# Performance work log

Measured on AMD Instinct MI355X. Metric: run time of the kernel, lower is better.

## Reference

```python
import jax, jax.numpy as jnp
import numpy as np

N_NODES = 100000
N_EDGES = 1600000
IN_DIM = 256
OUT_DIM = 128


def setup_inputs() -> dict:
    key = jax.random.key(0)
    k1, k2, k3, k4, k5 = jax.random.split(key, 5)
    h = jax.random.normal(k1, (N_NODES, IN_DIM), dtype=jnp.float32)
    # xavier_normal-ish scales for the two weight matrices
    W = jax.random.normal(k2, (IN_DIM, OUT_DIM), dtype=jnp.float32) * (2.0 / np.sqrt(IN_DIM + OUT_DIM))
    a = jax.random.normal(k3, (2 * OUT_DIM,), dtype=jnp.float32) * (2.0 / np.sqrt(2 * OUT_DIM + 1))
    src = jax.random.randint(k4, (N_EDGES,), 0, N_NODES, dtype=jnp.int32)
    dst = jax.random.randint(k5, (N_EDGES,), 0, N_NODES, dtype=jnp.int32)
    return {"h": h, "W": W, "a": a, "src": src, "dst": dst}


def reference(h, W, a, src, dst):
    n = h.shape[0]
    d = W.shape[1]
    z = h @ W  # [N, out_dim]
    # attn_fc([z_src || z_dst]) == z_src @ a[:d] + z_dst @ a[d:]
    el = z @ a[:d]  # [N]
    er = z @ a[d:]  # [N]
    e = jax.nn.leaky_relu(el[src] + er[dst])  # [E], torch default slope 0.01
    # per-destination (segment) softmax, numerically stable
    seg_max = jax.ops.segment_max(e, dst, num_segments=n)
    e_exp = jnp.exp(e - seg_max[dst])
    denom = jax.ops.segment_sum(e_exp, dst, num_segments=n)
    alpha = e_exp / denom[dst]  # [E]
    # weighted scatter-sum of source z into destinations
    h_out = jax.ops.segment_sum(alpha[:, None] * z[src], dst, num_segments=n)
    return h_out
```

## Files before the change

kernel.cpp:

```cpp
#include <hip/hip_runtime.h>
#include <cstdint>
#include <cstddef>

#define N_NODES 100000
#define N_EDGES 1600000
#define IN_DIM  256
#define OUT_DIM 128

#define BSHIFT 7
#define BNODES 128
#define NBUCK  782
#define BCAP   3200
#define MAXE   13
#define EPB    2048

#define ENC_NEG_INF 0x00800000u

typedef __attribute__((ext_vector_type(8))) short bf16x8;
typedef __attribute__((ext_vector_type(4))) float f32x4;

__device__ __forceinline__ unsigned bf16rn(float f) {
    unsigned u = __float_as_uint(f);
    return (u + 0x7FFFu + ((u >> 16) & 1u)) >> 16;
}

__global__ void w16s_k(const float* __restrict__ W, unsigned short* __restrict__ w16s,
                       int* __restrict__ bucket_cursor)
{
    int t = blockIdx.x * blockDim.x + threadIdx.x;
    if (t < NBUCK) bucket_cursor[t] = 0;
    if (t >= IN_DIM * OUT_DIM) return;
    int j  = t & 7;
    int n  = (t >> 3) & 15;
    int q  = (t >> 7) & 3;
    int c  = (t >> 9) & 7;
    int kc = t >> 12;
    int k   = kc * 32 + q * 8 + j;
    int dim = (c >> 1) * 32 + n * 2 + (c & 1);
    w16s[t] = (unsigned short)bf16rn(W[k * OUT_DIM + dim]);
}

#define LA_STRIDE 264

__global__ __launch_bounds__(256) void gemm_z_k(
    const float* __restrict__ h, const unsigned short* __restrict__ w16s,
    const float* __restrict__ a,
    unsigned short* __restrict__ z16, float* __restrict__ el, float* __restrict__ er)
{
    __shared__ unsigned short lA[64 * LA_STRIDE];
    const int t  = threadIdx.x;
    const int n0 = blockIdx.x * 64;

    #pragma unroll
    for (int p = 0; p < 16; ++p) {
        int f = p * 256 + t;
        int i = f >> 6;
        int col = (f & 63) * 4;
        float4 v = make_float4(0.f, 0.f, 0.f, 0.f);
        if (n0 + i < N_NODES)
            v = *(const float4*)&h[(size_t)(n0 + i) * IN_DIM + col];
        uint2 pk;
        pk.x = bf16rn(v.x) | (bf16rn(v.y) << 16);
        pk.y = bf16rn(v.z) | (bf16rn(v.w) << 16);
        *(uint2*)&lA[i * LA_STRIDE + col] = pk;
    }
    __syncthreads();

    const int w    = t >> 6;
    const int lane = t & 63;
    const int q    = lane >> 4;
    const int col  = lane & 15;

    f32x4 acc[8];
    #pragma unroll
    for (int c = 0; c < 8; ++c) acc[c] = (f32x4){0.f, 0.f, 0.f, 0.f};

    #pragma unroll
    for (int kc = 0; kc < 8; ++kc) {
        bf16x8 af = *(const bf16x8*)&lA[(w * 16 + col) * LA_STRIDE + kc * 32 + q * 8];
        bf16x8 bfr[8];
        #pragma unroll
        for (int c = 0; c < 8; ++c)
            bfr[c] = *(const bf16x8*)&w16s[((((kc * 8 + c) * 4 + q) * 16) + col) * 8];
        #pragma unroll
        for (int c = 0; c < 8; ++c)
            acc[c] = __builtin_amdgcn_mfma_f32_16x16x32_bf16(af, bfr[c], acc[c], 0, 0, 0);
    }

    float aL[8], aR[8];
    #pragma unroll
    for (int c = 0; c < 8; ++c) {
        int dim = (c >> 1) * 32 + col * 2 + (c & 1);
        aL[c] = a[dim];
        aR[c] = a[128 + dim];
    }
    #pragma unroll
    for (int r = 0; r < 4; ++r) {
        int node = n0 + w * 16 + q * 4 + r;
        float sl = 0.f, sr = 0.f;
        #pragma unroll
        for (int c = 0; c < 8; ++c) {
            sl += acc[c][r] * aL[c];
            sr += acc[c][r] * aR[c];
        }
        #pragma unroll
        for (int o = 1; o < 16; o <<= 1) {
            sl += __shfl_xor(sl, o, 64);
            sr += __shfl_xor(sr, o, 64);
        }
        if (node < N_NODES) {
            #pragma unroll
            for (int g = 0; g < 4; ++g) {
                unsigned u = bf16rn(acc[2 * g][r]) | (bf16rn(acc[2 * g + 1][r]) << 16);
                ((unsigned*)z16)[(size_t)node * 64 + g * 16 + col] = u;
            }
            if (col == 0) { el[node] = sl; er[node] = sr; }
        }
    }
}

__global__ __launch_bounds__(256) void partition_k(
    const int* __restrict__ src, const int* __restrict__ dst,
    const float* __restrict__ el, const float* __restrict__ er,
    int* __restrict__ bucket_cursor, unsigned long long* __restrict__ ebuf)
{
    __shared__ int hist[NBUCK];
    __shared__ int gbaseL[NBUCK];
    const int t = threadIdx.x;
    for (int i = t; i < NBUCK; i += 256) hist[i] = 0;
    __syncthreads();

    const int e0 = blockIdx.x * EPB;
    int bucks[8], ranks[8];
    unsigned long long pk[8];
    #pragma unroll
    for (int k = 0; k < 8; ++k) {
        int e = e0 + k * 256 + t;
        bucks[k] = -1;
        if (e < N_EDGES) {
            int s = src[e], d = dst[e];
            float v = el[s] + er[d];
            v = (v > 0.0f) ? v : 0.01f * v;
            int b = d >> BSHIFT;
            bucks[k] = b;
            ranks[k] = atomicAdd(&hist[b], 1);
            pk[k] = ((unsigned long long)__float_as_uint(v) << 32)
                  | ((unsigned)s << BSHIFT) | (unsigned)(d & (BNODES - 1));
        }
    }
    __syncthreads();
    for (int i = t; i < NBUCK; i += 256) {
        int hc = hist[i];
        gbaseL[i] = hc ? atomicAdd(&bucket_cursor[i], hc) : 0;
    }
    __syncthreads();
    #pragma unroll
    for (int k = 0; k < 8; ++k)
        if (bucks[k] >= 0)
            ebuf[(size_t)bucks[k] * BCAP + gbaseL[bucks[k]] + ranks[k]] = pk[k];
}

__global__ __launch_bounds__(256) void bucket_k(
    const int* __restrict__ bucket_cursor, const unsigned long long* __restrict__ ebuf,
    unsigned long long* __restrict__ perm, int* __restrict__ begA, int* __restrict__ endA)
{
    __shared__ int deg[BNODES];
    __shared__ int off[BNODES];
    __shared__ unsigned emaxL[BNODES];
    __shared__ int ssum[BNODES];

    const int b = blockIdx.x;
    const int t = threadIdx.x;
    const int cnt = bucket_cursor[b];
    const unsigned long long* eb = ebuf + (size_t)b * BCAP;
    unsigned long long* pb = perm + (size_t)b * BCAP;

    if (t < BNODES) { deg[t] = 0; emaxL[t] = ENC_NEG_INF; }
    __syncthreads();

    unsigned long long pv[MAXE];
    int rk[MAXE];
    #pragma unroll
    for (int k = 0; k < MAXE; ++k) {
        int i = t + k * 256;
        if (i < cnt) {
            unsigned long long v = eb[i];
            int ld = (int)(v & (BNODES - 1));
            unsigned e32 = (unsigned)(v >> 32);
            unsigned enc = (e32 & 0x80000000u) ? ~e32 : (e32 | 0x80000000u);
            rk[k] = atomicAdd(&deg[ld], 1);
            atomicMax(&emaxL[ld], enc);
            pv[k] = v;
        }
    }
    __syncthreads();

    int d = 0, pd = 0;
    if (t < BNODES) {
        d  = deg[t];
        pd = (d + 3) & ~3;
        ssum[t] = pd;
    }
    __syncthreads();
    #pragma unroll
    for (int o = 1; o < BNODES; o <<= 1) {
        int v = 0;
        if (t >= o && t < BNODES) v = ssum[t - o];
        __syncthreads();
        if (t < BNODES) ssum[t] += v;
        __syncthreads();
    }
    if (t < BNODES) off[t] = ssum[t] - pd;
    __syncthreads();

    #pragma unroll
    for (int k = 0; k < MAXE; ++k) {
        int i = t + k * 256;
        if (i < cnt) {
            unsigned long long v = pv[k];
            int ld = (int)(v & (BNODES - 1));
            unsigned s = (unsigned)((v >> BSHIFT) & 0x1FFFFu);
            float e = __uint_as_float((unsigned)(v >> 32));
            unsigned u = emaxL[ld];
            float mx = (u & 0x80000000u) ? __uint_as_float(u ^ 0x80000000u)
                                         : __uint_as_float(~u);
            float w = __expf(e - mx);
            pb[off[ld] + rk[k]] = ((unsigned long long)__float_as_uint(w) << 32) | s;
        }
    }

    if (t < BNODES) {
        int n = b * BNODES + t;
        if (n < N_NODES) {
            int o  = off[t];
            int gb = b * BCAP + o;
            begA[n] = gb;
            endA[n] = gb + pd;
            for (int j = o + d; j < o + pd; ++j) pb[j] = 0ull;
        }
    }
}

__global__ __launch_bounds__(256) void node_pass_k(
    const int* __restrict__ begA, const int* __restrict__ endA,
    const unsigned long long* __restrict__ perm,
    const unsigned* __restrict__ z16, float* __restrict__ out)
{
    int n    = (blockIdx.x * blockDim.x + threadIdx.x) >> 6;
    int lane = threadIdx.x & 63;
    if (n >= N_NODES) return;
    int beg = begA[n], end = endA[n];

    float acc0 = 0.0f, acc1 = 0.0f;
    if (end > beg) {
        float dsum = 0.0f;
        const uint4* pp = (const uint4*)perm;
        #pragma unroll 2
        for (int i = (beg >> 2); i < (end >> 2); ++i) {
            uint4 pA = pp[2 * i];
            uint4 pB = pp[2 * i + 1];
            unsigned q0 = z16[(size_t)pA.x * 64 + lane];
            unsigned q1 = z16[(size_t)pA.z * 64 + lane];
            unsigned q2 = z16[(size_t)pB.x * 64 + lane];
            unsigned q3 = z16[(size_t)pB.z * 64 + lane];
            float w0 = __uint_as_float(pA.y);
            float w1 = __uint_as_float(pA.w);
            float w2 = __uint_as_float(pB.y);
            float w3 = __uint_as_float(pB.w);
            acc0 += w0 * __uint_as_float(q0 << 16)
                  + w1 * __uint_as_float(q1 << 16)
                  + w2 * __uint_as_float(q2 << 16)
                  + w3 * __uint_as_float(q3 << 16);
            acc1 += w0 * __uint_as_float(q0 & 0xFFFF0000u)
                  + w1 * __uint_as_float(q1 & 0xFFFF0000u)
                  + w2 * __uint_as_float(q2 & 0xFFFF0000u)
                  + w3 * __uint_as_float(q3 & 0xFFFF0000u);
            dsum += w0 + w1 + w2 + w3;
        }
        float inv = 1.0f / dsum;
        acc0 *= inv; acc1 *= inv;
    }
    *(float2*)&out[(size_t)n * OUT_DIM + lane * 2] = make_float2(acc0, acc1);
}

extern "C" void kernel_launch(void* const* d_in, const int* in_sizes, int n_in,
                              void* d_out, int out_size, void* d_ws, size_t ws_size,
                              hipStream_t stream)
{
    (void)in_sizes; (void)n_in; (void)out_size; (void)ws_size;
    const float* h = (const float*)d_in[0];
    const float* W = (const float*)d_in[1];
    const float* a = (const float*)d_in[2];
    const int* src = (const int*)d_in[3];
    const int* dst = (const int*)d_in[4];
    float* out = (float*)d_out;

    char* ws = (char*)d_ws;
    size_t off = 0;
    auto alloc = [&](size_t bytes) -> char* {
        char* p = ws + off;
        off += (bytes + 255) & ~(size_t)255;
        return p;
    };
    unsigned short* z16  = (unsigned short*)alloc((size_t)N_NODES * OUT_DIM * 2);
    unsigned short* w16s = (unsigned short*)alloc((size_t)IN_DIM * OUT_DIM * 2);
    float*    el        = (float*)   alloc((size_t)N_NODES * 4);
    float*    er        = (float*)   alloc((size_t)N_NODES * 4);
    int*      bucket_cursor = (int*) alloc((size_t)NBUCK * 4);
    unsigned long long* ebuf = (unsigned long long*)alloc((size_t)NBUCK * BCAP * 8);
    unsigned long long* perm = (unsigned long long*)alloc((size_t)NBUCK * BCAP * 8);
    int*      begA      = (int*)     alloc((size_t)N_NODES * 4);
    int*      endA      = (int*)     alloc((size_t)N_NODES * 4);

    w16s_k<<<(IN_DIM * OUT_DIM + 255) / 256, 256, 0, stream>>>(W, w16s, bucket_cursor);
    gemm_z_k<<<(N_NODES + 63) / 64, 256, 0, stream>>>(h, w16s, a, z16, el, er);
    partition_k<<<(N_EDGES + EPB - 1) / EPB, 256, 0, stream>>>(src, dst, el, er,
                                                               bucket_cursor, ebuf);
    bucket_k<<<NBUCK, 256, 0, stream>>>(bucket_cursor, ebuf, perm, begA, endA);
    node_pass_k<<<(N_NODES * 64 + 255) / 256, 256, 0, stream>>>(begA, endA, perm,
                                                                (const unsigned*)z16, out);
}
```

Baseline: 314.2 us.

## Build destination CSR via global degree scan and atomic scatter

Replaces the two-level bucket partition (per-block histograms, bucket buffer, per-bucket sort) with a global CSR build. Per-destination degrees are counted with global atomics, prefix-scanned in two levels, and edges are then scattered into padded rows using an atomic cursor, with the segment max tracked by an atomicMax on an order-preserving encoding. The exp(e - max) is moved into the node aggregation pass, which removes the bucket kernel and its intermediate buffer. The GEMM also drops its LDS staging and loads and converts h straight into MFMA fragments. In exchange, each edge now needs several random global atomics and a scattered write, each lane recomputes the exp, and edge order within a row becomes nondeterministic.

Result: slower. 468.4 us (+49.1%).

```diff
diff --git a/kernel.cpp b/kernel.cpp
--- a/kernel.cpp
+++ b/kernel.cpp
@@ -7,14 +7,8 @@
 #define IN_DIM  256
 #define OUT_DIM 128
 
-#define BSHIFT 7
-#define BNODES 128
-#define NBUCK  782
-#define BCAP   3200
-#define MAXE   13
-#define EPB    2048
-
-#define ENC_NEG_INF 0x00800000u
+#define NSB 391
+#define PERM_CAP (N_EDGES + 4 * N_NODES)
 
 typedef __attribute__((ext_vector_type(8))) short bf16x8;
 typedef __attribute__((ext_vector_type(4))) float f32x4;
@@ -24,11 +18,12 @@
     return (u + 0x7FFFu + ((u >> 16) & 1u)) >> 16;
 }
 
-__global__ void w16s_k(const float* __restrict__ W, unsigned short* __restrict__ w16s,
-                       int* __restrict__ bucket_cursor)
+__global__ __launch_bounds__(256) void setup_k(
+    const float* __restrict__ W, unsigned short* __restrict__ w16s,
+    int* __restrict__ deg, unsigned* __restrict__ emaxEnc)
 {
     int t = blockIdx.x * blockDim.x + threadIdx.x;
-    if (t < NBUCK) bucket_cursor[t] = 0;
+    if (t < N_NODES) { deg[t] = 0; emaxEnc[t] = 0u; }
     if (t >= IN_DIM * OUT_DIM) return;
     int j  = t & 7;
     int n  = (t >> 3) & 15;
@@ -40,51 +35,107 @@
     w16s[t] = (unsigned short)bf16rn(W[k * OUT_DIM + dim]);
 }
 
-#define LA_STRIDE 264
+__global__ __launch_bounds__(256) void deg_k(const int* __restrict__ dst,
+                                             int* __restrict__ deg)
+{
+    int e0 = blockIdx.x * 1024 + threadIdx.x;
+    #pragma unroll
+    for (int k = 0; k < 4; ++k) {
+        int e = e0 + k * 256;
+        if (e < N_EDGES) atomicAdd(&deg[dst[e]], 1);
+    }
+}
+
+__global__ __launch_bounds__(256) void scan1_k(const int* __restrict__ deg,
+                                               int* __restrict__ nodeoff,
+                                               int* __restrict__ blocksum)
+{
+    __shared__ int s[256];
+    int b = blockIdx.x, t = threadIdx.x;
+    int n = b * 256 + t;
+    int d  = (n < N_NODES) ? deg[n] : 0;
+    int pd = (d + 3) & ~3;
+    s[t] = pd;
+    __syncthreads();
+    #pragma unroll
+    for (int o = 1; o < 256; o <<= 1) {
+        int v = (t >= o) ? s[t - o] : 0;
+        __syncthreads();
+        s[t] += v;
+        __syncthreads();
+    }
+    if (n < N_NODES) nodeoff[n] = s[t] - pd;
+    if (t == 255) blocksum[b] = s[255];
+}
+
+__global__ __launch_bounds__(512) void scan2_k(int* __restrict__ blocksum)
+{
+    __shared__ int s[512];
+    int t = threadIdx.x;
+    int v = (t < NSB) ? blocksum[t] : 0;
+    s[t] = v;
+    __syncthreads();
+    #pragma unroll
+    for (int o = 1; o < 512; o <<= 1) {
+        int x = (t >= o) ? s[t - o] : 0;
+        __syncthreads();
+        s[t] += x;
+        __syncthreads();
+    }
+    if (t < NSB) blocksum[t] = s[t] - v;
+}
+
+__global__ __launch_bounds__(256) void fixup_k(
+    const int* __restrict__ deg, const int* __restrict__ nodeoff,
+    const int* __restrict__ blocksum, int* __restrict__ begA, int* __restrict__ endA,
+    int* __restrict__ cur, unsigned long long* __restrict__ perm)
+{
+    int n = blockIdx.x * 256 + threadIdx.x;
+    if (n >= N_NODES) return;
+    int d  = deg[n];
+    int pd = (d + 3) & ~3;
+    int base = blocksum[n >> 8] + nodeoff[n];
+    begA[n] = base;
+    cur[n]  = base;
+    endA[n] = base + pd;
+    unsigned long long padv = ((unsigned long long)__float_as_uint(-1e30f)) << 32;
+    for (int j = base + d; j < base + pd; ++j) perm[j] = padv;
+}
 
 __global__ __launch_bounds__(256) void gemm_z_k(
     const float* __restrict__ h, const unsigned short* __restrict__ w16s,
     const float* __restrict__ a,
     unsigned short* __restrict__ z16, float* __restrict__ el, float* __restrict__ er)
 {
-    __shared__ unsigned short lA[64 * LA_STRIDE];
-    const int t  = threadIdx.x;
-    const int n0 = blockIdx.x * 64;
-
-    #pragma unroll
-    for (int p = 0; p < 16; ++p) {
-        int f = p * 256 + t;
-        int i = f >> 6;
-        int col = (f & 63) * 4;
-        float4 v = make_float4(0.f, 0.f, 0.f, 0.f);
-        if (n0 + i < N_NODES)
-            v = *(const float4*)&h[(size_t)(n0 + i) * IN_DIM + col];
-        uint2 pk;
-        pk.x = bf16rn(v.x) | (bf16rn(v.y) << 16);
-        pk.y = bf16rn(v.z) | (bf16rn(v.w) << 16);
-        *(uint2*)&lA[i * LA_STRIDE + col] = pk;
-    }
-    __syncthreads();
-
+    const int t    = threadIdx.x;
+    const int n0   = blockIdx.x * 64;
     const int w    = t >> 6;
     const int lane = t & 63;
     const int q    = lane >> 4;
     const int col  = lane & 15;
 
+    int row  = n0 + w * 16 + col;
+    int lrow = (row < N_NODES) ? row : (N_NODES - 1);
+    const float* hp = h + (size_t)lrow * IN_DIM + q * 8;
+
     f32x4 acc[8];
     #pragma unroll
     for (int c = 0; c < 8; ++c) acc[c] = (f32x4){0.f, 0.f, 0.f, 0.f};
 
     #pragma unroll
     for (int kc = 0; kc < 8; ++kc) {
-        bf16x8 af = *(const bf16x8*)&lA[(w * 16 + col) * LA_STRIDE + kc * 32 + q * 8];
-        bf16x8 bfr[8];
+        float4 v0 = *(const float4*)(hp + kc * 32);
+        float4 v1 = *(const float4*)(hp + kc * 32 + 4);
+        bf16x8 af;
+        af[0] = (short)bf16rn(v0.x); af[1] = (short)bf16rn(v0.y);
+        af[2] = (short)bf16rn(v0.z); af[3] = (short)bf16rn(v0.w);
+        af[4] = (short)bf16rn(v1.x); af[5] = (short)bf16rn(v1.y);
+        af[6] = (short)bf16rn(v1.z); af[7] = (short)bf16rn(v1.w);
         #pragma unroll
-        for (int c = 0; c < 8; ++c)
-            bfr[c] = *(const bf16x8*)&w16s[((((kc * 8 + c) * 4 + q) * 16) + col) * 8];
-        #pragma unroll
-        for (int c = 0; c < 8; ++c)
-            acc[c] = __builtin_amdgcn_mfma_f32_16x16x32_bf16(af, bfr[c], acc[c], 0, 0, 0);
+        for (int c = 0; c < 8; ++c) {
+            bf16x8 bfr = *(const bf16x8*)&w16s[((((kc * 8 + c) * 4 + q) * 16) + col) * 8];
+            acc[c] = __builtin_amdgcn_mfma_f32_16x16x32_bf16(af, bfr, acc[c], 0, 0, 0);
+        }
     }
 
     float aL[8], aR[8];
@@ -119,131 +170,32 @@
     }
 }
 
-__global__ __launch_bounds__(256) void partition_k(
+__global__ __launch_bounds__(256) void scatter_k(
     const int* __restrict__ src, const int* __restrict__ dst,
     const float* __restrict__ el, const float* __restrict__ er,
-    int* __restrict__ bucket_cursor, unsigned long long* __restrict__ ebuf)
-{
-    __shared__ int hist[NBUCK];
-    __shared__ int gbaseL[NBUCK];
-    const int t = threadIdx.x;
-    for (int i = t; i < NBUCK; i += 256) hist[i] = 0;
-    __syncthreads();
-
-    const int e0 = blockIdx.x * EPB;
-    int bucks[8], ranks[8];
-    unsigned long long pk[8];
-    #pragma unroll
-    for (int k = 0; k < 8; ++k) {
-        int e = e0 + k * 256 + t;
-        bucks[k] = -1;
+    int* __restrict__ cur, unsigned* __restrict__ emaxEnc,
+    unsigned long long* __restrict__ perm)
+{
+    int e0 = blockIdx.x * 1024 + threadIdx.x;
+    #pragma unroll
+    for (int k = 0; k < 4; ++k) {
+        int e = e0 + k * 256;
         if (e < N_EDGES) {
             int s = src[e], d = dst[e];
             float v = el[s] + er[d];
             v = (v > 0.0f) ? v : 0.01f * v;
-            int b = d >> BSHIFT;
-            bucks[k] = b;
-            ranks[k] = atomicAdd(&hist[b], 1);
-            pk[k] = ((unsigned long long)__float_as_uint(v) << 32)
-                  | ((unsigned)s << BSHIFT) | (unsigned)(d & (BNODES - 1));
-        }
-    }
-    __syncthreads();
-    for (int i = t; i < NBUCK; i += 256) {
-        int hc = hist[i];
-        gbaseL[i] = hc ? atomicAdd(&bucket_cursor[i], hc) : 0;
-    }
-    __syncthreads();
-    #pragma unroll
-    for (int k = 0; k < 8; ++k)
-        if (bucks[k] >= 0)
-            ebuf[(size_t)bucks[k] * BCAP + gbaseL[bucks[k]] + ranks[k]] = pk[k];
-}
-
-__global__ __launch_bounds__(256) void bucket_k(
-    const int* __restrict__ bucket_cursor, const unsigned long long* __restrict__ ebuf,
-    unsigned long long* __restrict__ perm, int* __restrict__ begA, int* __restrict__ endA)
-{
-    __shared__ int deg[BNODES];
-    __shared__ int off[BNODES];
-    __shared__ unsigned emaxL[BNODES];
-    __shared__ int ssum[BNODES];
-
-    const int b = blockIdx.x;
-    const int t = threadIdx.x;
-    const int cnt = bucket_cursor[b];
-    const unsigned long long* eb = ebuf + (size_t)b * BCAP;
-    unsigned long long* pb = perm + (size_t)b * BCAP;
-
-    if (t < BNODES) { deg[t] = 0; emaxL[t] = ENC_NEG_INF; }
-    __syncthreads();
-
-    unsigned long long pv[MAXE];
-    int rk[MAXE];
-    #pragma unroll
-    for (int k = 0; k < MAXE; ++k) {
-        int i = t + k * 256;
-        if (i < cnt) {
-            unsigned long long v = eb[i];
-            int ld = (int)(v & (BNODES - 1));
-            unsigned e32 = (unsigned)(v >> 32);
-            unsigned enc = (e32 & 0x80000000u) ? ~e32 : (e32 | 0x80000000u);
-            rk[k] = atomicAdd(&deg[ld], 1);
-            atomicMax(&emaxL[ld], enc);
-            pv[k] = v;
-        }
-    }
-    __syncthreads();
-
-    int d = 0, pd = 0;
-    if (t < BNODES) {
-        d  = deg[t];
-        pd = (d + 3) & ~3;
-        ssum[t] = pd;
-    }
-    __syncthreads();
-    #pragma unroll
-    for (int o = 1; o < BNODES; o <<= 1) {
-        int v = 0;
-        if (t >= o && t < BNODES) v = ssum[t - o];
-        __syncthreads();
-        if (t < BNODES) ssum[t] += v;
-        __syncthreads();
-    }
-    if (t < BNODES) off[t] = ssum[t] - pd;
-    __syncthreads();
-
-    #pragma unroll
-    for (int k = 0; k < MAXE; ++k) {
-        int i = t + k * 256;
-        if (i < cnt) {
-            unsigned long long v = pv[k];
-            int ld = (int)(v & (BNODES - 1));
-            unsigned s = (unsigned)((v >> BSHIFT) & 0x1FFFFu);
-            float e = __uint_as_float((unsigned)(v >> 32));
-            unsigned u = emaxL[ld];
-            float mx = (u & 0x80000000u) ? __uint_as_float(u ^ 0x80000000u)
-                                         : __uint_as_float(~u);
-            float w = __expf(e - mx);
-            pb[off[ld] + rk[k]] = ((unsigned long long)__float_as_uint(w) << 32) | s;
-        }
-    }
-
-    if (t < BNODES) {
-        int n = b * BNODES + t;
-        if (n < N_NODES) {
-            int o  = off[t];
-            int gb = b * BCAP + o;
-            begA[n] = gb;
-            endA[n] = gb + pd;
-            for (int j = o + d; j < o + pd; ++j) pb[j] = 0ull;
+            unsigned u = __float_as_uint(v);
+            unsigned enc = (u >> 31) ? ~u : (u | 0x80000000u);
+            atomicMax(&emaxEnc[d], enc);
+            int p = atomicAdd(&cur[d], 1);
+            perm[(size_t)p] = ((unsigned long long)u << 32) | (unsigned)s;
         }
     }
 }
 
 __global__ __launch_bounds__(256) void node_pass_k(
     const int* __restrict__ begA, const int* __restrict__ endA,
-    const unsigned long long* __restrict__ perm,
+    const unsigned* __restrict__ emaxEnc, const unsigned long long* __restrict__ perm,
     const unsigned* __restrict__ z16, float* __restrict__ out)
 {
     int n    = (blockIdx.x * blockDim.x + threadIdx.x) >> 6;
@@ -253,6 +205,9 @@
 
     float acc0 = 0.0f, acc1 = 0.0f;
     if (end > beg) {
+        unsigned um = emaxEnc[n];
+        float mx = (um & 0x80000000u) ? __uint_as_float(um ^ 0x80000000u)
+                                      : __uint_as_float(~um);
         float dsum = 0.0f;
         const uint4* pp = (const uint4*)perm;
         #pragma unroll 2
@@ -263,10 +218,10 @@
             unsigned q1 = z16[(size_t)pA.z * 64 + lane];
             unsigned q2 = z16[(size_t)pB.x * 64 + lane];
             unsigned q3 = z16[(size_t)pB.z * 64 + lane];
-            float w0 = __uint_as_float(pA.y);
-            float w1 = __uint_as_float(pA.w);
-            float w2 = __uint_as_float(pB.y);
-            float w3 = __uint_as_float(pB.w);
+            float w0 = __expf(__uint_as_float(pA.y) - mx);
+            float w1 = __expf(__uint_as_float(pA.w) - mx);
+            float w2 = __expf(__uint_as_float(pB.y) - mx);
+            float w3 = __expf(__uint_as_float(pB.w) - mx);
             acc0 += w0 * __uint_as_float(q0 << 16)
                   + w1 * __uint_as_float(q1 << 16)
                   + w2 * __uint_as_float(q2 << 16)
@@ -306,17 +261,25 @@
     unsigned short* w16s = (unsigned short*)alloc((size_t)IN_DIM * OUT_DIM * 2);
     float*    el        = (float*)   alloc((size_t)N_NODES * 4);
     float*    er        = (float*)   alloc((size_t)N_NODES * 4);
-    int*      bucket_cursor = (int*) alloc((size_t)NBUCK * 4);
-    unsigned long long* ebuf = (unsigned long long*)alloc((size_t)NBUCK * BCAP * 8);
-    unsigned long long* perm = (unsigned long long*)alloc((size_t)NBUCK * BCAP * 8);
+    int*      deg       = (int*)     alloc((size_t)N_NODES * 4);
+    int*      nodeoff   = (int*)     alloc((size_t)N_NODES * 4);
+    int*      blocksum  = (int*)     alloc((size_t)NSB * 4);
     int*      begA      = (int*)     alloc((size_t)N_NODES * 4);
     int*      endA      = (int*)     alloc((size_t)N_NODES * 4);
-
-    w16s_k<<<(IN_DIM * OUT_DIM + 255) / 256, 256, 0, stream>>>(W, w16s, bucket_cursor);
+    int*      cur       = (int*)     alloc((size_t)N_NODES * 4);
+    unsigned* emaxEnc   = (unsigned*)alloc((size_t)N_NODES * 4);
+    unsigned long long* perm = (unsigned long long*)alloc((size_t)PERM_CAP * 8);
+
+    setup_k<<<(N_NODES + 255) / 256, 256, 0, stream>>>(W, w16s, deg, emaxEnc);
+    deg_k<<<(N_EDGES + 1023) / 1024, 256, 0, stream>>>(dst, deg);
+    scan1_k<<<NSB, 256, 0, stream>>>(deg, nodeoff, blocksum);
+    scan2_k<<<1, 512, 0, stream>>>(blocksum);
+    fixup_k<<<(N_NODES + 255) / 256, 256, 0, stream>>>(deg, nodeoff, blocksum,
+                                                       begA, endA, cur, perm);
     gemm_z_k<<<(N_NODES + 63) / 64, 256, 0, stream>>>(h, w16s, a, z16, el, er);
-    partition_k<<<(N_EDGES + EPB - 1) / EPB, 256, 0, stream>>>(src, dst, el, er,
-                                                               bucket_cursor, ebuf);
-    bucket_k<<<NBUCK, 256, 0, stream>>>(bucket_cursor, ebuf, perm, begA, endA);
-    node_pass_k<<<(N_NODES * 64 + 255) / 256, 256, 0, stream>>>(begA, endA, perm,
-                                                                (const unsigned*)z16, out);
-}
+    scatter_k<<<(N_EDGES + 1023) / 1024, 256, 0, stream>>>(src, dst, el, er,
+                                                           cur, emaxEnc, perm);
+    node_pass_k<<<(N_NODES * 64 + 255) / 256, 256, 0, stream>>>(begA, endA, emaxEnc,
+                                                                perm, (const unsigned*)z16,
+                                                                out);
+}
```

## Fuse bucket sort with node aggregation in LDS and defer edge scores

Applied to the files above, without the earlier changes.

Merges the bucket-sort and node-pass kernels so each bucket's sorted weights and source indices stay in shared memory instead of round-tripping through global perm/beg/end arrays. Edge scores are now computed from el/er inside the fused kernel, which halves the partition buffer width and lets partition run before the GEMM. The GEMM reads h directly into registers without LDS staging, and the prefix scan uses wave shuffles. The trade-off is much lower parallelism in the gather phase: each wave aggregates 32 nodes serially across only 782 blocks.

Result: no change. 308.3 us (-1.9%).

```diff
diff --git a/kernel.cpp b/kernel.cpp
--- a/kernel.cpp
+++ b/kernel.cpp
@@ -13,6 +13,7 @@
 #define BCAP   3200
 #define MAXE   13
 #define EPB    2048
+#define LCAP   3584
 
 #define ENC_NEG_INF 0x00800000u
 
@@ -23,9 +24,18 @@
     unsigned u = __float_as_uint(f);
     return (u + 0x7FFFu + ((u >> 16) & 1u)) >> 16;
 }
-
-__global__ void w16s_k(const float* __restrict__ W, unsigned short* __restrict__ w16s,
-                       int* __restrict__ bucket_cursor)
+__device__ __forceinline__ unsigned encOrd(float e) {
+    unsigned u = __float_as_uint(e);
+    return (u >> 31) ? ~u : (u | 0x80000000u);
+}
+__device__ __forceinline__ float decOrd(unsigned um) {
+    return (um & 0x80000000u) ? __uint_as_float(um ^ 0x80000000u)
+                              : __uint_as_float(~um);
+}
+
+__global__ __launch_bounds__(256) void setup_k(
+    const float* __restrict__ W, unsigned short* __restrict__ w16s,
+    int* __restrict__ bucket_cursor)
 {
     int t = blockIdx.x * blockDim.x + threadIdx.x;
     if (t < NBUCK) bucket_cursor[t] = 0;
@@ -40,51 +50,77 @@
     w16s[t] = (unsigned short)bf16rn(W[k * OUT_DIM + dim]);
 }
 
-#define LA_STRIDE 264
+__global__ __launch_bounds__(256) void partition_k(
+    const int* __restrict__ src, const int* __restrict__ dst,
+    int* __restrict__ bucket_cursor, unsigned* __restrict__ ebuf)
+{
+    __shared__ int hist[NBUCK];
+    __shared__ int gbaseL[NBUCK];
+    const int t = threadIdx.x;
+    for (int i = t; i < NBUCK; i += 256) hist[i] = 0;
+    __syncthreads();
+
+    const int e0 = blockIdx.x * EPB;
+    int bucks[8], ranks[8];
+    unsigned pk[8];
+    #pragma unroll
+    for (int k = 0; k < 8; ++k) {
+        int e = e0 + k * 256 + t;
+        bucks[k] = -1;
+        if (e < N_EDGES) {
+            int s = src[e], d = dst[e];
+            int b = d >> BSHIFT;
+            bucks[k] = b;
+            ranks[k] = atomicAdd(&hist[b], 1);
+            pk[k] = ((unsigned)s << BSHIFT) | (unsigned)(d & (BNODES - 1));
+        }
+    }
+    __syncthreads();
+    for (int i = t; i < NBUCK; i += 256) {
+        int hc = hist[i];
+        gbaseL[i] = hc ? atomicAdd(&bucket_cursor[i], hc) : 0;
+    }
+    __syncthreads();
+    #pragma unroll
+    for (int k = 0; k < 8; ++k)
+        if (bucks[k] >= 0)
+            ebuf[(size_t)bucks[k] * BCAP + gbaseL[bucks[k]] + ranks[k]] = pk[k];
+}
 
 __global__ __launch_bounds__(256) void gemm_z_k(
     const float* __restrict__ h, const unsigned short* __restrict__ w16s,
     const float* __restrict__ a,
     unsigned short* __restrict__ z16, float* __restrict__ el, float* __restrict__ er)
 {
-    __shared__ unsigned short lA[64 * LA_STRIDE];
-    const int t  = threadIdx.x;
-    const int n0 = blockIdx.x * 64;
-
-    #pragma unroll
-    for (int p = 0; p < 16; ++p) {
-        int f = p * 256 + t;
-        int i = f >> 6;
-        int col = (f & 63) * 4;
-        float4 v = make_float4(0.f, 0.f, 0.f, 0.f);
-        if (n0 + i < N_NODES)
-            v = *(const float4*)&h[(size_t)(n0 + i) * IN_DIM + col];
-        uint2 pk;
-        pk.x = bf16rn(v.x) | (bf16rn(v.y) << 16);
-        pk.y = bf16rn(v.z) | (bf16rn(v.w) << 16);
-        *(uint2*)&lA[i * LA_STRIDE + col] = pk;
-    }
-    __syncthreads();
-
+    const int t    = threadIdx.x;
+    const int n0   = blockIdx.x * 64;
     const int w    = t >> 6;
     const int lane = t & 63;
     const int q    = lane >> 4;
     const int col  = lane & 15;
 
+    int row  = n0 + w * 16 + col;
+    int lrow = (row < N_NODES) ? row : (N_NODES - 1);
+    const float* hp = h + (size_t)lrow * IN_DIM + q * 8;
+
     f32x4 acc[8];
     #pragma unroll
     for (int c = 0; c < 8; ++c) acc[c] = (f32x4){0.f, 0.f, 0.f, 0.f};
 
     #pragma unroll
     for (int kc = 0; kc < 8; ++kc) {
-        bf16x8 af = *(const bf16x8*)&lA[(w * 16 + col) * LA_STRIDE + kc * 32 + q * 8];
-        bf16x8 bfr[8];
+        float4 v0 = *(const float4*)(hp + kc * 32);
+        float4 v1 = *(const float4*)(hp + kc * 32 + 4);
+        bf16x8 af;
+        af[0] = (short)bf16rn(v0.x); af[1] = (short)bf16rn(v0.y);
+        af[2] = (short)bf16rn(v0.z); af[3] = (short)bf16rn(v0.w);
+        af[4] = (short)bf16rn(v1.x); af[5] = (short)bf16rn(v1.y);
+        af[6] = (short)bf16rn(v1.z); af[7] = (short)bf16rn(v1.w);
         #pragma unroll
-        for (int c = 0; c < 8; ++c)
-            bfr[c] = *(const bf16x8*)&w16s[((((kc * 8 + c) * 4 + q) * 16) + col) * 8];
-        #pragma unroll
-        for (int c = 0; c < 8; ++c)
-            acc[c] = __builtin_amdgcn_mfma_f32_16x16x32_bf16(af, bfr[c], acc[c], 0, 0, 0);
+        for (int c = 0; c < 8; ++c) {
+            bf16x8 bfr = *(const bf16x8*)&w16s[((((kc * 8 + c) * 4 + q) * 16) + col) * 8];
+            acc[c] = __builtin_amdgcn_mfma_f32_16x16x32_bf16(af, bfr, acc[c], 0, 0, 0);
+        }
     }
 
     float aL[8], aR[8];
@@ -119,154 +155,101 @@
     }
 }
 
-__global__ __launch_bounds__(256) void partition_k(
-    const int* __restrict__ src, const int* __restrict__ dst,
+__global__ __launch_bounds__(256) void bucket_node_k(
+    const int* __restrict__ bucket_cursor, const unsigned* __restrict__ ebuf,
     const float* __restrict__ el, const float* __restrict__ er,
-    int* __restrict__ bucket_cursor, unsigned long long* __restrict__ ebuf)
-{
-    __shared__ int hist[NBUCK];
-    __shared__ int gbaseL[NBUCK];
-    const int t = threadIdx.x;
-    for (int i = t; i < NBUCK; i += 256) hist[i] = 0;
-    __syncthreads();
-
-    const int e0 = blockIdx.x * EPB;
-    int bucks[8], ranks[8];
-    unsigned long long pk[8];
-    #pragma unroll
-    for (int k = 0; k < 8; ++k) {
-        int e = e0 + k * 256 + t;
-        bucks[k] = -1;
-        if (e < N_EDGES) {
-            int s = src[e], d = dst[e];
-            float v = el[s] + er[d];
-            v = (v > 0.0f) ? v : 0.01f * v;
-            int b = d >> BSHIFT;
-            bucks[k] = b;
-            ranks[k] = atomicAdd(&hist[b], 1);
-            pk[k] = ((unsigned long long)__float_as_uint(v) << 32)
-                  | ((unsigned)s << BSHIFT) | (unsigned)(d & (BNODES - 1));
-        }
-    }
-    __syncthreads();
-    for (int i = t; i < NBUCK; i += 256) {
-        int hc = hist[i];
-        gbaseL[i] = hc ? atomicAdd(&bucket_cursor[i], hc) : 0;
-    }
-    __syncthreads();
-    #pragma unroll
-    for (int k = 0; k < 8; ++k)
-        if (bucks[k] >= 0)
-            ebuf[(size_t)bucks[k] * BCAP + gbaseL[bucks[k]] + ranks[k]] = pk[k];
-}
-
-__global__ __launch_bounds__(256) void bucket_k(
-    const int* __restrict__ bucket_cursor, const unsigned long long* __restrict__ ebuf,
-    unsigned long long* __restrict__ perm, int* __restrict__ begA, int* __restrict__ endA)
-{
-    __shared__ int deg[BNODES];
-    __shared__ int off[BNODES];
+    const unsigned* __restrict__ z16, float* __restrict__ out)
+{
+    __shared__ float    erL[BNODES];
+    __shared__ int      deg[BNODES];
+    __shared__ int      off[BNODES];
     __shared__ unsigned emaxL[BNODES];
-    __shared__ int ssum[BNODES];
+    __shared__ int      wvSum[4];
+    __shared__ float    wL[LCAP];
+    __shared__ int      sL[LCAP];
 
     const int b = blockIdx.x;
     const int t = threadIdx.x;
-    const int cnt = bucket_cursor[b];
-    const unsigned long long* eb = ebuf + (size_t)b * BCAP;
-    unsigned long long* pb = perm + (size_t)b * BCAP;
-
-    if (t < BNODES) { deg[t] = 0; emaxL[t] = ENC_NEG_INF; }
-    __syncthreads();
-
-    unsigned long long pv[MAXE];
-    int rk[MAXE];
+    int cnt = bucket_cursor[b];
+    if (cnt > BCAP) cnt = BCAP;
+    const unsigned* eb = ebuf + (size_t)b * BCAP;
+
+    if (t < BNODES) {
+        deg[t] = 0; emaxL[t] = ENC_NEG_INF;
+        int n = b * BNODES + t;
+        erL[t] = (n < N_NODES) ? er[n] : 0.f;
+    }
+    __syncthreads();
+
+    unsigned pv[MAXE]; int rk[MAXE]; float ev[MAXE];
     #pragma unroll
     for (int k = 0; k < MAXE; ++k) {
         int i = t + k * 256;
         if (i < cnt) {
-            unsigned long long v = eb[i];
+            unsigned v = eb[i];
+            int s  = (int)(v >> BSHIFT);
             int ld = (int)(v & (BNODES - 1));
-            unsigned e32 = (unsigned)(v >> 32);
-            unsigned enc = (e32 & 0x80000000u) ? ~e32 : (e32 | 0x80000000u);
+            float e = el[s] + erL[ld];
+            e = (e > 0.0f) ? e : 0.01f * e;
             rk[k] = atomicAdd(&deg[ld], 1);
-            atomicMax(&emaxL[ld], enc);
-            pv[k] = v;
-        }
-    }
-    __syncthreads();
-
-    int d = 0, pd = 0;
+            atomicMax(&emaxL[ld], encOrd(e));
+            pv[k] = v; ev[k] = e;
+        }
+    }
+    __syncthreads();
+
+    int d = 0, pd = 0, incl = 0;
     if (t < BNODES) {
         d  = deg[t];
         pd = (d + 3) & ~3;
-        ssum[t] = pd;
-    }
-    __syncthreads();
-    #pragma unroll
-    for (int o = 1; o < BNODES; o <<= 1) {
-        int v = 0;
-        if (t >= o && t < BNODES) v = ssum[t - o];
-        __syncthreads();
-        if (t < BNODES) ssum[t] += v;
-        __syncthreads();
-    }
-    if (t < BNODES) off[t] = ssum[t] - pd;
+        incl = pd;
+    }
+    #pragma unroll
+    for (int o = 1; o < 64; o <<= 1) {
+        int x = __shfl_up(incl, o, 64);
+        if ((t & 63) >= o) incl += x;
+    }
+    if (t < BNODES && (t & 63) == 63) wvSum[t >> 6] = incl;
+    __syncthreads();
+    if (t < BNODES) off[t] = ((t >= 64) ? wvSum[0] : 0) + incl - pd;
     __syncthreads();
 
     #pragma unroll
     for (int k = 0; k < MAXE; ++k) {
         int i = t + k * 256;
         if (i < cnt) {
-            unsigned long long v = pv[k];
-            int ld = (int)(v & (BNODES - 1));
-            unsigned s = (unsigned)((v >> BSHIFT) & 0x1FFFFu);
-            float e = __uint_as_float((unsigned)(v >> 32));
-            unsigned u = emaxL[ld];
-            float mx = (u & 0x80000000u) ? __uint_as_float(u ^ 0x80000000u)
-                                         : __uint_as_float(~u);
-            float w = __expf(e - mx);
-            pb[off[ld] + rk[k]] = ((unsigned long long)__float_as_uint(w) << 32) | s;
-        }
-    }
-
+            int ld = (int)(pv[k] & (BNODES - 1));
+            float mx = decOrd(emaxL[ld]);
+            int p = off[ld] + rk[k];
+            wL[p] = __expf(ev[k] - mx);
+            sL[p] = (int)(pv[k] >> BSHIFT);
+        }
+    }
     if (t < BNODES) {
-        int n = b * BNODES + t;
-        if (n < N_NODES) {
-            int o  = off[t];
-            int gb = b * BCAP + o;
-            begA[n] = gb;
-            endA[n] = gb + pd;
-            for (int j = o + d; j < o + pd; ++j) pb[j] = 0ull;
-        }
-    }
-}
-
-__global__ __launch_bounds__(256) void node_pass_k(
-    const int* __restrict__ begA, const int* __restrict__ endA,
-    const unsigned long long* __restrict__ perm,
-    const unsigned* __restrict__ z16, float* __restrict__ out)
-{
-    int n    = (blockIdx.x * blockDim.x + threadIdx.x) >> 6;
-    int lane = threadIdx.x & 63;
-    if (n >= N_NODES) return;
-    int beg = begA[n], end = endA[n];
-
-    float acc0 = 0.0f, acc1 = 0.0f;
-    if (end > beg) {
-        float dsum = 0.0f;
-        const uint4* pp = (const uint4*)perm;
-        #pragma unroll 2
-        for (int i = (beg >> 2); i < (end >> 2); ++i) {
-            uint4 pA = pp[2 * i];
-            uint4 pB = pp[2 * i + 1];
-            unsigned q0 = z16[(size_t)pA.x * 64 + lane];
-            unsigned q1 = z16[(size_t)pA.z * 64 + lane];
-            unsigned q2 = z16[(size_t)pB.x * 64 + lane];
-            unsigned q3 = z16[(size_t)pB.z * 64 + lane];
-            float w0 = __uint_as_float(pA.y);
-            float w1 = __uint_as_float(pA.w);
-            float w2 = __uint_as_float(pB.y);
-            float w3 = __uint_as_float(pB.w);
+        int o = off[t];
+        for (int j = o + d; j < o + pd; ++j) { wL[j] = 0.0f; sL[j] = 0; }
+    }
+    __syncthreads();
+
+    const int wv   = t >> 6;
+    const int lane = t & 63;
+    for (int k = 0; k < BNODES / 4; ++k) {
+        int ln = wv * (BNODES / 4) + k;
+        int n  = b * BNODES + ln;
+        if (n >= N_NODES) break;
+        int o   = off[ln];
+        int dl  = deg[ln];
+        int pdl = (dl + 3) & ~3;
+        float acc0 = 0.f, acc1 = 0.f, dsum = 0.f;
+        for (int i = o; i < o + pdl; i += 4) {
+            float w0 = wL[i],     w1 = wL[i + 1];
+            float w2 = wL[i + 2], w3 = wL[i + 3];
+            int   s0 = sL[i],     s1 = sL[i + 1];
+            int   s2 = sL[i + 2], s3 = sL[i + 3];
+            unsigned q0 = z16[(size_t)s0 * 64 + lane];
+            unsigned q1 = z16[(size_t)s1 * 64 + lane];
+            unsigned q2 = z16[(size_t)s2 * 64 + lane];
+            unsigned q3 = z16[(size_t)s3 * 64 + lane];
             acc0 += w0 * __uint_as_float(q0 << 16)
                   + w1 * __uint_as_float(q1 << 16)
                   + w2 * __uint_as_float(q2 << 16)
@@ -277,10 +260,12 @@
                   + w3 * __uint_as_float(q3 & 0xFFFF0000u);
             dsum += w0 + w1 + w2 + w3;
         }
-        float inv = 1.0f / dsum;
-        acc0 *= inv; acc1 *= inv;
-    }
-    *(float2*)&out[(size_t)n * OUT_DIM + lane * 2] = make_float2(acc0, acc1);
+        if (pdl > 0) {
+            float inv = 1.0f / dsum;
+            acc0 *= inv; acc1 *= inv;
+        }
+        *(float2*)&out[(size_t)n * OUT_DIM + lane * 2] = make_float2(acc0, acc1);
+    }
 }
 
 extern "C" void kernel_launch(void* const* d_in, const int* in_sizes, int n_in,
@@ -307,16 +292,12 @@
     float*    el        = (float*)   alloc((size_t)N_NODES * 4);
     float*    er        = (float*)   alloc((size_t)N_NODES * 4);
     int*      bucket_cursor = (int*) alloc((size_t)NBUCK * 4);
-    unsigned long long* ebuf = (unsigned long long*)alloc((size_t)NBUCK * BCAP * 8);
-    unsigned long long* perm = (unsigned long long*)alloc((size_t)NBUCK * BCAP * 8);
-    int*      begA      = (int*)     alloc((size_t)N_NODES * 4);
-    int*      endA      = (int*)     alloc((size_t)N_NODES * 4);
-
-    w16s_k<<<(IN_DIM * OUT_DIM + 255) / 256, 256, 0, stream>>>(W, w16s, bucket_cursor);
+    unsigned* ebuf      = (unsigned*)alloc((size_t)NBUCK * BCAP * 4);
+
+    setup_k<<<(IN_DIM * OUT_DIM + 255) / 256, 256, 0, stream>>>(W, w16s, bucket_cursor);
+    partition_k<<<(N_EDGES + EPB - 1) / EPB, 256, 0, stream>>>(src, dst,
+                                                               bucket_cursor, ebuf);
     gemm_z_k<<<(N_NODES + 63) / 64, 256, 0, stream>>>(h, w16s, a, z16, el, er);
-    partition_k<<<(N_EDGES + EPB - 1) / EPB, 256, 0, stream>>>(src, dst, el, er,
-                                                               bucket_cursor, ebuf);
-    bucket_k<<<NBUCK, 256, 0, stream>>>(bucket_cursor, ebuf, perm, begA, endA);
-    node_pass_k<<<(N_NODES * 64 + 255) / 256, 256, 0, stream>>>(begA, endA, perm,
-                                                                (const unsigned*)z16, out);
-}
+    bucket_node_k<<<NBUCK, 256, 0, stream>>>(bucket_cursor, ebuf, el, er,
+                                             (const unsigned*)z16, out);
+}
```
